# Performance work log

Measured on AMD Instinct MI355X. Metric: run time of the kernel, lower is better.

The kernel has to match this reference:

```python
import jax, jax.numpy as jnp
import numpy as np

NUM_CODES = 1024
CODE_DIM = 64
N_TOKENS = 131072
DECAY = 0.99
EPS = 1e-5


def setup_inputs() -> dict:
    key = jax.random.key(0)
    k1, k2, k3, k4 = jax.random.split(key, 4)
    return {
        "z": jax.random.normal(k1, (N_TOKENS, CODE_DIM), dtype=jnp.float32),
        "codebook": jax.random.normal(k2, (NUM_CODES, CODE_DIM), dtype=jnp.float32),
        "cluster_size": jax.random.uniform(k3, (NUM_CODES,), dtype=jnp.float32),
        "ema_w": jax.random.normal(k4, (NUM_CODES, CODE_DIM), dtype=jnp.float32),
    }


def reference(z, codebook, cluster_size, ema_w):
    # Squared L2 distances; argmin over squared distances == argmin over cdist.
    # d2: [N, K]
    d2 = (
        jnp.sum(z * z, axis=-1, keepdims=True)
        - 2.0 * (z @ codebook.T)
        + jnp.sum(codebook * codebook, axis=-1)
    )
    indices = jnp.argmin(d2, axis=-1)          # [N] int
    quantized = codebook[indices]              # [N, D]

    # EMA statistics (torch version uses one_hot; segment_sum is the fused
    # equivalent without materializing the [N, K] one-hot matrix).
    counts = jax.ops.segment_sum(jnp.ones_like(indices, dtype=z.dtype), indices,
                                 num_segments=NUM_CODES)          # encodings.sum(0)
    dw = jax.ops.segment_sum(z, indices, num_segments=NUM_CODES)  # encodings.T @ z

    new_cluster_size = DECAY * cluster_size + (1.0 - DECAY) * counts
    new_ema_w = DECAY * ema_w + (1.0 - DECAY) * dw
    n = jnp.sum(new_cluster_size)
    cs = (new_cluster_size + EPS) / (n + NUM_CODES * EPS) * n
    new_codebook = new_ema_w / cs[:, None]

    commitment_loss = jnp.mean((z - jax.lax.stop_gradient(quantized)) ** 2)
    quantized_st = z + jax.lax.stop_gradient(quantized - z)  # straight-through

    return quantized_st, indices, commitment_loss, new_codebook, new_cluster_size, new_ema_w
```

## Files before the change

### kernel.cpp

```cpp
#include <hip/hip_runtime.h>
#include <hip/hip_bf16.h>


#define DECAY 0.99f
#define OMD   0.01f
#define EPSV  1e-5f
#define BIASF 192.0f

typedef __attribute__((ext_vector_type(8))) __bf16 bf16x8;
typedef __attribute__((ext_vector_type(4))) float  float4v;

static __device__ __forceinline__ unsigned short bfbits(float f) {
    __bf16 h = (__bf16)f;
    return __builtin_bit_cast(unsigned short, h);
}
static __device__ __forceinline__ bf16x8 cvt8(float4v a, float4v b) {
    bf16x8 r;
    r[0] = (__bf16)a[0]; r[1] = (__bf16)a[1]; r[2] = (__bf16)a[2]; r[3] = (__bf16)a[3];
    r[4] = (__bf16)b[0]; r[5] = (__bf16)b[1]; r[6] = (__bf16)b[2]; r[7] = (__bf16)b[3];
    return r;
}

static __device__ __forceinline__ int dec_idx(unsigned key, int quad) {
    int iter = key & 255;
    return ((iter >> 6) << 8) + (((iter >> 2) & 15) << 4) + (quad << 2) + (iter & 3);
}

__global__ void vq_prep(const float* __restrict__ cb,
                        float* __restrict__ wsf, int* __restrict__ wsi,
                        int K, int NT) {
    int t = blockIdx.x * 256 + threadIdx.x;
    if (t < K) {
        wsi[t] = 0;
        const float4v* cp = (const float4v*)(cb + (size_t)t * 64);
        float s = 0.f;
        #pragma unroll
        for (int i = 0; i < 16; ++i) {
            float4v v = cp[i];
            s += v[0] * v[0] + v[1] * v[1] + v[2] * v[2] + v[3] * v[3];
        }
        wsf[K + t] = BIASF - 0.5f * s;
    }
    if (t == 0) wsf[2 * K] = 0.f;
}

__launch_bounds__(512)
__global__ void vq_main(const float* __restrict__ z,
                        const float* __restrict__ cb,
                        float* __restrict__ wsf, int* __restrict__ wsi,
                        float* __restrict__ out,
                        int NT, int K) {
    __shared__ __align__(16) unsigned short cbs[256 * 72];
    __shared__ float cns[256];
    __shared__ int hist[1024];

    const int tid  = threadIdx.x;
    const int lane = tid & 63;
    const int wave = tid >> 6;
    const int col  = lane & 15;
    const int quad = lane >> 4;
    const int wtok0 = blockIdx.x * 256 + wave * 32;
    const float* cnormp = wsf + K;
    float* lossp = wsf + 2 * K;
    const bool smallK = (K <= 1024);

    for (int i = tid; i < 1024; i += 512) hist[i] = 0;

    bf16x8 bf0[2], bf1[2];
    #pragma unroll
    for (int g = 0; g < 2; ++g) {
        int tok = wtok0 + g * 16 + col;
        if (tok >= NT) tok = NT - 1;
        const float* zp = z + (size_t)tok * 64 + quad * 8;
        float4v f0 = *(const float4v*)(zp);
        float4v f1 = *(const float4v*)(zp + 4);
        float4v f2 = *(const float4v*)(zp + 32);
        float4v f3 = *(const float4v*)(zp + 36);
        bf0[g] = cvt8(f0, f1);
        bf1[g] = cvt8(f2, f3);
    }

    unsigned k1[2] = { 0u, 0u }, k2[2] = { 0u, 0u };
    const unsigned kmask = 0xFFFFFF00u;
    const int nchunk = (K + 255) >> 8;

    for (int c = 0; c < nchunk; ++c) {
        #pragma unroll
        for (int i = 0; i < 8; ++i) {
            int f4 = (i * 512 + tid) * 4;
            int row = f4 >> 6, d = f4 & 63;
            int code = c * 256 + row;
            uint2 p;
            if (code < K) {
                float4v v = *(const float4v*)(cb + (size_t)code * 64 + d);
                p.x = (unsigned int)bfbits(v[0]) | ((unsigned int)bfbits(v[1]) << 16);
                p.y = (unsigned int)bfbits(v[2]) | ((unsigned int)bfbits(v[3]) << 16);
            } else { p.x = 0u; p.y = 0u; }
            *(uint2*)(&cbs[row * 72 + d]) = p;
        }
        if (tid < 256) {
            int code = c * 256 + tid;
            cns[tid] = (code < K) ? cnormp[code] : 0.0f;
        }
        __syncthreads();

        #pragma unroll 4
        for (int t = 0; t < 16; ++t) {
            const unsigned short* arow = cbs + (t * 16 + col) * 72;
            bf16x8 a0 = *(const bf16x8*)(arow + quad * 8);
            bf16x8 a1 = *(const bf16x8*)(arow + 32 + quad * 8);
            float4v cni = *(const float4v*)(cns + t * 16 + quad * 4);
            const int iterbase = (c << 6) | (t << 2);
            #pragma unroll
            for (int g = 0; g < 2; ++g) {
                float4v acc = cni;
                acc = __builtin_amdgcn_mfma_f32_16x16x32_bf16(a0, bf0[g], acc, 0, 0, 0);
                acc = __builtin_amdgcn_mfma_f32_16x16x32_bf16(a1, bf1[g], acc, 0, 0, 0);
                #pragma unroll
                for (int r = 0; r < 4; ++r) {
                    unsigned kb = (__float_as_uint(acc[r]) & kmask) | (unsigned)(iterbase + r);
                    unsigned lo = k2[g] > kb ? k2[g] : kb;
                    k2[g] = k1[g] < lo ? k1[g] : lo;
                    k1[g] = k1[g] > kb ? k1[g] : kb;
                }
            }
        }
        __syncthreads();
    }

    int ibst[2];
    #pragma unroll
    for (int g = 0; g < 2; ++g) {
        int tok = wtok0 + g * 16 + col;
        if (tok >= NT) tok = NT - 1;
        int ia = dec_idx(k1[g], quad);
        int ib = dec_idx(k2[g], quad);
        int cand[8];
        #pragma unroll
        for (int q = 0; q < 4; ++q) {
            cand[2 * q]     = __shfl(ia, q * 16 + col, 64);
            cand[2 * q + 1] = __shfl(ib, q * 16 + col, 64);
        }
        const float* zr = z + (size_t)tok * 64 + quad * 16;
        float4v zv0 = *(const float4v*)(zr);
        float4v zv1 = *(const float4v*)(zr + 4);
        float4v zv2 = *(const float4v*)(zr + 8);
        float4v zv3 = *(const float4v*)(zr + 12);
        double ps[8];
        #pragma unroll
        for (int s = 0; s < 8; ++s) {
            int cc = (cand[s] < K) ? cand[s] : 0;
            const float* cr = cb + (size_t)cc * 64 + quad * 16;
            float4v c0 = *(const float4v*)(cr);
            float4v c1 = *(const float4v*)(cr + 4);
            float4v c2 = *(const float4v*)(cr + 8);
            float4v c3 = *(const float4v*)(cr + 12);
            double a = 0.0;
            #pragma unroll
            for (int j = 0; j < 4; ++j) {
                double e0 = (double)zv0[j] - (double)c0[j];
                double e1 = (double)zv1[j] - (double)c1[j];
                double e2 = (double)zv2[j] - (double)c2[j];
                double e3 = (double)zv3[j] - (double)c3[j];
                a = fma(e0, e0, a); a = fma(e1, e1, a);
                a = fma(e2, e2, a); a = fma(e3, e3, a);
            }
            ps[s] = (cand[s] < K) ? a : 1.0e300;
        }
        #pragma unroll
        for (int s = 0; s < 8; ++s) {
            ps[s] += __shfl_xor(ps[s], 16, 64);
            ps[s] += __shfl_xor(ps[s], 32, 64);
        }
        double bs = ps[0]; int bi = cand[0];
        #pragma unroll
        for (int s = 1; s < 8; ++s) {
            if (ps[s] < bs || (ps[s] == bs && cand[s] < bi)) { bs = ps[s]; bi = cand[s]; }
        }
        ibst[g] = bi;
    }

    const size_t off_idx = (size_t)NT * 64;

    if (lane < 32) {
        int tk = wtok0 + lane;
        if (tk < NT) {
            int ib = (lane < 16) ? ibst[0] : ibst[1];
            out[off_idx + tk] = (float)ib;
            if (smallK) atomicAdd(&hist[ib], 1);
            else        atomicAdd(&wsi[ib], 1);
        }
    }

    float lsum = 0.f;
    #pragma unroll
    for (int i = 0; i < 8; ++i) {
        int tw  = i * 4 + quad;
        int g   = i >> 2;
        int idx = __shfl(ibst[g], tw & 15, 64);
        int token = wtok0 + tw;
        if (token < NT) {
            int d4 = col * 4;
            float4v zf = *(const float4v*)(z  + (size_t)token * 64 + d4);
            float4v qf = *(const float4v*)(cb + (size_t)idx   * 64 + d4);
            *(float4v*)(out + (size_t)token * 64 + d4) = qf;
            float e0 = zf[0] - qf[0], e1 = zf[1] - qf[1];
            float e2 = zf[2] - qf[2], e3 = zf[3] - qf[3];
            lsum += e0 * e0 + e1 * e1 + e2 * e2 + e3 * e3;
        }
    }
    #pragma unroll
    for (int off = 1; off < 64; off <<= 1) lsum += __shfl_xor(lsum, off, 64);
    if (lane == 0) atomicAdd(lossp, lsum);

    __syncthreads();
    if (smallK) {
        for (int k = tid; k < K; k += 512) {
            int c = hist[k];
            if (c) atomicAdd(&wsi[k], c);
        }
    }
}

__launch_bounds__(512)
__global__ void vq_dwred(const float* __restrict__ z,
                         const float* __restrict__ out_idx,
                         const float* __restrict__ cs,
                         float* __restrict__ wsf, const int* __restrict__ wsi,
                         float* __restrict__ partial,
                         float* __restrict__ out,
                         int NT, int K, int nchunks) {
    extern __shared__ float acc[];
    __shared__ float red[8];

    const int tid   = threadIdx.x;
    const int lane  = tid & 63;
    const int wave  = tid >> 6;
    const int chunk = blockIdx.x >> 2;
    const int g     = blockIdx.x & 3;
    const int tsub  = lane >> 4;
    const int d     = lane & 15;
    const size_t KD = (size_t)K * 64;

    for (int i = tid; i < K * 16; i += 512) acc[i] = 0.f;

    if (blockIdx.x == 0) {
        float part = 0.f;
        for (int k = tid; k < K; k += 512)
            part += DECAY * cs[k] + OMD * (float)wsi[k];
        #pragma unroll
        for (int off = 1; off < 64; off <<= 1) part += __shfl_xor(part, off, 64);
        if (lane == 0) red[wave] = part;
        __syncthreads();
        if (tid == 0) {
            float nn = 0.f;
            #pragma unroll
            for (int i = 0; i < 8; ++i) nn += red[i];
            wsf[2 * K + 1] = nn;
            out[(size_t)NT * 64 + NT] = wsf[2 * K] / ((float)NT * 64.0f);
        }
    }
    __syncthreads();

    const int C  = (NT + nchunks - 1) / nchunks;
    const int T0 = chunk * C;
    const int T1 = (T0 + C < NT) ? (T0 + C) : NT;
    const float* zs = z + g * 16 + d;

    #pragma unroll 4
    for (int t = T0 + wave * 4 + tsub; t < T1; t += 32) {
        float v   = zs[(size_t)t * 64];
        int  code = (int)out_idx[t];
        atomicAdd(&acc[code * 16 + d], v);
    }
    __syncthreads();

    float* pb = partial + (size_t)chunk * KD + g * 16;
    for (int i = tid; i < K * 16; i += 512) {
        int k = i >> 4, dd = i & 15;
        pb[(size_t)k * 64 + dd] = acc[i];
    }
}

__global__ void vq_final(const float* __restrict__ cs,
                         const float* __restrict__ ema,
                         const float* __restrict__ wsf,
                         const int* __restrict__ wsi,
                         const float* __restrict__ partial,
                         float* __restrict__ out, int NT, int K, int S) {
    const int KD = K * 64;
    int t = blockIdx.x * 256 + threadIdx.x;
    if (t >= KD) return;
    const int k = t >> 6;
    const float n = wsf[2 * K + 1];
    float dsum = 0.f;
    #pragma unroll 4
    for (int s = 0; s < S; ++s) dsum += partial[(size_t)s * KD + t];
    const float dw = DECAY * ema[t] + OMD * dsum;
    const float ncs = DECAY * cs[k] + OMD * (float)wsi[k];
    const float csn = (ncs + EPSV) / (n + (float)K * EPSV) * n;
    const size_t off_cb  = (size_t)NT * 64 + NT + 1;
    const size_t off_cs  = off_cb + (size_t)KD;
    const size_t off_ema = off_cs + K;
    out[off_cb  + t] = dw / csn;
    out[off_ema + t] = dw;
    if ((t & 63) == 0) out[off_cs + k] = ncs;
}

extern "C" void kernel_launch(void* const* d_in, const int* in_sizes, int n_in,
                              void* d_out, int out_size, void* d_ws, size_t ws_size,
                              hipStream_t stream) {
    const float* z   = (const float*)d_in[0];
    const float* cb  = (const float*)d_in[1];
    const float* cs  = (const float*)d_in[2];
    const float* ema = (const float*)d_in[3];
    float* out = (float*)d_out;
    float* wsf = (float*)d_ws;
    int*   wsi = (int*)d_ws;

    const int NT = in_sizes[0] / 64;
    const int K  = in_sizes[2];
    const int KD = K * 64;

    size_t avail = ws_size / 4;
    int nchunks = 128;
    while (nchunks > 1 && (size_t)2 * K + 2 + (size_t)nchunks * KD > avail)
        nchunks >>= 1;

    float* partial = wsf + 2 * K + 2;
    const size_t dwlds = (size_t)K * 16 * sizeof(float);

    vq_prep<<<(K + 255) / 256, 256, 0, stream>>>(cb, wsf, wsi, K, NT);
    vq_main<<<(NT + 255) / 256, 512, 0, stream>>>(z, cb, wsf, wsi, out, NT, K);
    vq_dwred<<<nchunks * 4, 512, dwlds, stream>>>(
        z, out + (size_t)NT * 64, cs, wsf, wsi, partial, out, NT, K, nchunks);
    vq_final<<<(KD + 255) / 256, 256, 0, stream>>>(cs, ema, wsf, wsi, partial,
                                                   out, NT, K, nchunks);
}
```

Before: 247.6 us.

## Pre-pack bf16 codebook MFMA fragments in prep kernel, read directly from global

The prep kernel now converts the codebook to bf16 once and stores it in the exact per-lane MFMA fragment layout in workspace. The main kernel drops its LDS staging of the codebook and norms, along with the per-chunk barriers, and loads each fragment straight from global/L2 inside the distance loop. This removes redundant per-block fp32-to-bf16 conversion and LDS traffic. In exchange, every wave now streams the packed codebook from cache with no LDS reuse, so the loop depends on L2 bandwidth and latency.

```diff
diff --git a/kernel.cpp b/kernel.cpp
--- a/kernel.cpp
+++ b/kernel.cpp
@@ -10,10 +10,6 @@
 typedef __attribute__((ext_vector_type(8))) __bf16 bf16x8;
 typedef __attribute__((ext_vector_type(4))) float  float4v;
 
-static __device__ __forceinline__ unsigned short bfbits(float f) {
-    __bf16 h = (__bf16)f;
-    return __builtin_bit_cast(unsigned short, h);
-}
 static __device__ __forceinline__ bf16x8 cvt8(float4v a, float4v b) {
     bf16x8 r;
     r[0] = (__bf16)a[0]; r[1] = (__bf16)a[1]; r[2] = (__bf16)a[2]; r[3] = (__bf16)a[3];
@@ -28,6 +24,7 @@
 
 __global__ void vq_prep(const float* __restrict__ cb,
                         float* __restrict__ wsf, int* __restrict__ wsi,
+                        unsigned short* __restrict__ pk,
                         int K, int NT) {
     int t = blockIdx.x * 256 + threadIdx.x;
     if (t < K) {
@@ -41,25 +38,41 @@
         }
         wsf[K + t] = BIASF - 0.5f * s;
     }
+    if (t < K * 4) {
+        int tg  = t >> 6;
+        int l   = t & 63;
+        int col = l & 15, q = l >> 4;
+        int code = tg * 16 + col;
+        bf16x8 a0, a1;
+        if (code < K) {
+            const float* s0 = cb + (size_t)code * 64 + q * 8;
+            a0 = cvt8(*(const float4v*)(s0),      *(const float4v*)(s0 + 4));
+            a1 = cvt8(*(const float4v*)(s0 + 32), *(const float4v*)(s0 + 36));
+        } else {
+            #pragma unroll
+            for (int j = 0; j < 8; ++j) { a0[j] = (__bf16)0.f; a1[j] = (__bf16)0.f; }
+        }
+        bf16x8* dst = (bf16x8*)(pk + (size_t)t * 16);
+        dst[0] = a0;
+        dst[1] = a1;
+    }
     if (t == 0) wsf[2 * K] = 0.f;
 }
 
 __launch_bounds__(512)
 __global__ void vq_main(const float* __restrict__ z,
                         const float* __restrict__ cb,
+                        const unsigned short* __restrict__ pk,
                         float* __restrict__ wsf, int* __restrict__ wsi,
                         float* __restrict__ out,
                         int NT, int K) {
-    __shared__ __align__(16) unsigned short cbs[256 * 72];
-    __shared__ float cns[256];
     __shared__ int hist[1024];
 
     const int tid  = threadIdx.x;
     const int lane = tid & 63;
-    const int wave = tid >> 6;
     const int col  = lane & 15;
     const int quad = lane >> 4;
-    const int wtok0 = blockIdx.x * 256 + wave * 32;
+    const int wtok0 = blockIdx.x * 256 + (tid >> 6) * 32;
     const float* cnormp = wsf + K;
     float* lossp = wsf + 2 * K;
     const bool smallK = (K <= 1024);
@@ -72,60 +85,35 @@
         int tok = wtok0 + g * 16 + col;
         if (tok >= NT) tok = NT - 1;
         const float* zp = z + (size_t)tok * 64 + quad * 8;
-        float4v f0 = *(const float4v*)(zp);
-        float4v f1 = *(const float4v*)(zp + 4);
-        float4v f2 = *(const float4v*)(zp + 32);
-        float4v f3 = *(const float4v*)(zp + 36);
-        bf0[g] = cvt8(f0, f1);
-        bf1[g] = cvt8(f2, f3);
+        bf0[g] = cvt8(*(const float4v*)(zp),      *(const float4v*)(zp + 4));
+        bf1[g] = cvt8(*(const float4v*)(zp + 32), *(const float4v*)(zp + 36));
     }
 
     unsigned k1[2] = { 0u, 0u }, k2[2] = { 0u, 0u };
     const unsigned kmask = 0xFFFFFF00u;
-    const int nchunk = (K + 255) >> 8;
-
-    for (int c = 0; c < nchunk; ++c) {
-        #pragma unroll
-        for (int i = 0; i < 8; ++i) {
-            int f4 = (i * 512 + tid) * 4;
-            int row = f4 >> 6, d = f4 & 63;
-            int code = c * 256 + row;
-            uint2 p;
-            if (code < K) {
-                float4v v = *(const float4v*)(cb + (size_t)code * 64 + d);
-                p.x = (unsigned int)bfbits(v[0]) | ((unsigned int)bfbits(v[1]) << 16);
-                p.y = (unsigned int)bfbits(v[2]) | ((unsigned int)bfbits(v[3]) << 16);
-            } else { p.x = 0u; p.y = 0u; }
-            *(uint2*)(&cbs[row * 72 + d]) = p;
-        }
-        if (tid < 256) {
-            int code = c * 256 + tid;
-            cns[tid] = (code < K) ? cnormp[code] : 0.0f;
-        }
-        __syncthreads();
-
-        #pragma unroll 4
-        for (int t = 0; t < 16; ++t) {
-            const unsigned short* arow = cbs + (t * 16 + col) * 72;
-            bf16x8 a0 = *(const bf16x8*)(arow + quad * 8);
-            bf16x8 a1 = *(const bf16x8*)(arow + 32 + quad * 8);
-            float4v cni = *(const float4v*)(cns + t * 16 + quad * 4);
-            const int iterbase = (c << 6) | (t << 2);
+    const int ngrp = (K + 15) >> 4;
+    const unsigned short* pl = pk + lane * 16;
+
+    #pragma unroll 2
+    for (int tt = 0; tt < ngrp; ++tt) {
+        const bf16x8* frag = (const bf16x8*)(pl + (size_t)tt * 1024);
+        bf16x8 a0 = frag[0];
+        bf16x8 a1 = frag[1];
+        float4v cni = *(const float4v*)(cnormp + tt * 16 + quad * 4);
+        const int iterbase = tt << 2;
+        #pragma unroll
+        for (int g = 0; g < 2; ++g) {
+            float4v acc = cni;
+            acc = __builtin_amdgcn_mfma_f32_16x16x32_bf16(a0, bf0[g], acc, 0, 0, 0);
+            acc = __builtin_amdgcn_mfma_f32_16x16x32_bf16(a1, bf1[g], acc, 0, 0, 0);
             #pragma unroll
-            for (int g = 0; g < 2; ++g) {
-                float4v acc = cni;
-                acc = __builtin_amdgcn_mfma_f32_16x16x32_bf16(a0, bf0[g], acc, 0, 0, 0);
-                acc = __builtin_amdgcn_mfma_f32_16x16x32_bf16(a1, bf1[g], acc, 0, 0, 0);
-                #pragma unroll
-                for (int r = 0; r < 4; ++r) {
-                    unsigned kb = (__float_as_uint(acc[r]) & kmask) | (unsigned)(iterbase + r);
-                    unsigned lo = k2[g] > kb ? k2[g] : kb;
-                    k2[g] = k1[g] < lo ? k1[g] : lo;
-                    k1[g] = k1[g] > kb ? k1[g] : kb;
-                }
+            for (int r = 0; r < 4; ++r) {
+                unsigned kb = (__float_as_uint(acc[r]) & kmask) | (unsigned)(iterbase + r);
+                unsigned lo = k2[g] > kb ? k2[g] : kb;
+                k2[g] = k1[g] < lo ? k1[g] : lo;
+                k1[g] = k1[g] > kb ? k1[g] : kb;
             }
         }
-        __syncthreads();
     }
 
     int ibst[2];
@@ -181,6 +169,7 @@
     }
 
     const size_t off_idx = (size_t)NT * 64;
+    __syncthreads();
 
     if (lane < 32) {
         int tk = wtok0 + lane;
@@ -322,16 +311,20 @@
     const int K  = in_sizes[2];
     const int KD = K * 64;
 
+    const size_t off_pk = (((size_t)2 * K + 2) + 7) & ~(size_t)7;
+    const size_t off_pa = off_pk + (size_t)K * 32;
+
     size_t avail = ws_size / 4;
     int nchunks = 128;
-    while (nchunks > 1 && (size_t)2 * K + 2 + (size_t)nchunks * KD > avail)
+    while (nchunks > 1 && off_pa + (size_t)nchunks * KD > avail)
         nchunks >>= 1;
 
-    float* partial = wsf + 2 * K + 2;
+    unsigned short* pk = (unsigned short*)(wsf + off_pk);
+    float* partial = wsf + off_pa;
     const size_t dwlds = (size_t)K * 16 * sizeof(float);
 
-    vq_prep<<<(K + 255) / 256, 256, 0, stream>>>(cb, wsf, wsi, K, NT);
-    vq_main<<<(NT + 255) / 256, 512, 0, stream>>>(z, cb, wsf, wsi, out, NT, K);
+    vq_prep<<<(K * 4 + 255) / 256, 256, 0, stream>>>(cb, wsf, wsi, pk, K, NT);
+    vq_main<<<(NT + 255) / 256, 512, 0, stream>>>(z, cb, pk, wsf, wsi, out, NT, K);
     vq_dwred<<<nchunks * 4, 512, dwlds, stream>>>(
         z, out + (size_t)NT * 64, cs, wsf, wsi, partial, out, NT, K, nchunks);
     vq_final<<<(KD + 255) / 256, 256, 0, stream>>>(cs, ema, wsf, wsi, partial,
```

Result: slower. 255.8 us (+3.3%).

## Split quantized gather and loss into separate kernel; unroll partial reduction

Applied to the files above, without the earlier changes.

The gather of codebook rows into the quantized output and the commitment-loss accumulation move out of the distance/argmin kernel into a new elementwise kernel. That kernel reads the stored indices and uses 1024-thread blocks with a block-level reduction before one atomic. The intent is to shorten the argmin kernel and lower its register and latency pressure, while giving the gather a fully coalesced layout. It costs an extra launch and a re-read of z and the indices. The final reduction over partial sums also switches to eight independent accumulators to expose more memory-level parallelism.

```diff
diff --git a/kernel.cpp b/kernel.cpp
--- a/kernel.cpp
+++ b/kernel.cpp
@@ -45,11 +45,11 @@
 }
 
 __launch_bounds__(512)
-__global__ void vq_main(const float* __restrict__ z,
-                        const float* __restrict__ cb,
-                        float* __restrict__ wsf, int* __restrict__ wsi,
-                        float* __restrict__ out,
-                        int NT, int K) {
+__global__ void vq_assign(const float* __restrict__ z,
+                          const float* __restrict__ cb,
+                          float* __restrict__ wsf, int* __restrict__ wsi,
+                          float* __restrict__ out,
+                          int NT, int K) {
     __shared__ __align__(16) unsigned short cbs[256 * 72];
     __shared__ float cns[256];
     __shared__ int hist[1024];
@@ -61,7 +61,6 @@
     const int quad = lane >> 4;
     const int wtok0 = blockIdx.x * 256 + wave * 32;
     const float* cnormp = wsf + K;
-    float* lossp = wsf + 2 * K;
     const bool smallK = (K <= 1024);
 
     for (int i = tid; i < 1024; i += 512) hist[i] = 0;
@@ -192,33 +191,47 @@
         }
     }
 
-    float lsum = 0.f;
-    #pragma unroll
-    for (int i = 0; i < 8; ++i) {
-        int tw  = i * 4 + quad;
-        int g   = i >> 2;
-        int idx = __shfl(ibst[g], tw & 15, 64);
-        int token = wtok0 + tw;
-        if (token < NT) {
-            int d4 = col * 4;
-            float4v zf = *(const float4v*)(z  + (size_t)token * 64 + d4);
-            float4v qf = *(const float4v*)(cb + (size_t)idx   * 64 + d4);
-            *(float4v*)(out + (size_t)token * 64 + d4) = qf;
-            float e0 = zf[0] - qf[0], e1 = zf[1] - qf[1];
-            float e2 = zf[2] - qf[2], e3 = zf[3] - qf[3];
-            lsum += e0 * e0 + e1 * e1 + e2 * e2 + e3 * e3;
-        }
-    }
-    #pragma unroll
-    for (int off = 1; off < 64; off <<= 1) lsum += __shfl_xor(lsum, off, 64);
-    if (lane == 0) atomicAdd(lossp, lsum);
-
     __syncthreads();
     if (smallK) {
         for (int k = tid; k < K; k += 512) {
             int c = hist[k];
             if (c) atomicAdd(&wsi[k], c);
         }
+    }
+}
+
+__launch_bounds__(1024)
+__global__ void vq_quant(const float* __restrict__ z,
+                         const float* __restrict__ cb,
+                         const float* __restrict__ out_idx,
+                         float* __restrict__ out,
+                         float* __restrict__ lossp, int NT) {
+    __shared__ float red[16];
+    const int tid  = threadIdx.x;
+    const int lane = tid & 63;
+    const int wave = tid >> 6;
+    const int gt   = blockIdx.x * 1024 + tid;
+
+    float lsum = 0.f;
+    if (gt < NT * 16) {
+        int token = gt >> 4, seg = gt & 15;
+        int idx = (int)out_idx[token];
+        const float4v zf = *(const float4v*)(z  + (size_t)token * 64 + seg * 4);
+        const float4v qf = *(const float4v*)(cb + (size_t)idx   * 64 + seg * 4);
+        *(float4v*)(out + (size_t)token * 64 + seg * 4) = qf;
+        float e0 = zf[0] - qf[0], e1 = zf[1] - qf[1];
+        float e2 = zf[2] - qf[2], e3 = zf[3] - qf[3];
+        lsum = e0 * e0 + e1 * e1 + e2 * e2 + e3 * e3;
+    }
+    #pragma unroll
+    for (int off = 1; off < 64; off <<= 1) lsum += __shfl_xor(lsum, off, 64);
+    if (lane == 0) red[wave] = lsum;
+    __syncthreads();
+    if (tid == 0) {
+        float s = 0.f;
+        #pragma unroll
+        for (int i = 0; i < 16; ++i) s += red[i];
+        atomicAdd(lossp, s);
     }
 }
 
@@ -293,9 +306,21 @@
     if (t >= KD) return;
     const int k = t >> 6;
     const float n = wsf[2 * K + 1];
-    float dsum = 0.f;
-    #pragma unroll 4
-    for (int s = 0; s < S; ++s) dsum += partial[(size_t)s * KD + t];
+    float d0 = 0.f, d1 = 0.f, d2 = 0.f, d3 = 0.f;
+    float d4 = 0.f, d5 = 0.f, d6 = 0.f, d7 = 0.f;
+    int s = 0;
+    for (; s + 8 <= S; s += 8) {
+        d0 += partial[(size_t)(s + 0) * KD + t];
+        d1 += partial[(size_t)(s + 1) * KD + t];
+        d2 += partial[(size_t)(s + 2) * KD + t];
+        d3 += partial[(size_t)(s + 3) * KD + t];
+        d4 += partial[(size_t)(s + 4) * KD + t];
+        d5 += partial[(size_t)(s + 5) * KD + t];
+        d6 += partial[(size_t)(s + 6) * KD + t];
+        d7 += partial[(size_t)(s + 7) * KD + t];
+    }
+    for (; s < S; ++s) d0 += partial[(size_t)s * KD + t];
+    const float dsum = ((d0 + d1) + (d2 + d3)) + ((d4 + d5) + (d6 + d7));
     const float dw = DECAY * ema[t] + OMD * dsum;
     const float ncs = DECAY * cs[k] + OMD * (float)wsi[k];
     const float csn = (ncs + EPSV) / (n + (float)K * EPSV) * n;
@@ -331,7 +356,9 @@
     const size_t dwlds = (size_t)K * 16 * sizeof(float);
 
     vq_prep<<<(K + 255) / 256, 256, 0, stream>>>(cb, wsf, wsi, K, NT);
-    vq_main<<<(NT + 255) / 256, 512, 0, stream>>>(z, cb, wsf, wsi, out, NT, K);
+    vq_assign<<<(NT + 255) / 256, 512, 0, stream>>>(z, cb, wsf, wsi, out, NT, K);
+    vq_quant<<<(NT * 16 + 1023) / 1024, 1024, 0, stream>>>(
+        z, cb, out + (size_t)NT * 64, out, wsf + 2 * K, NT);
     vq_dwred<<<nchunks * 4, 512, dwlds, stream>>>(
         z, out + (size_t)NT * 64, cs, wsf, wsi, partial, out, NT, K, nchunks);
     vq_final<<<(KD + 255) / 256, 256, 0, stream>>>(cs, ema, wsf, wsi, partial,
```

New measurement: 242.2 us. 1.02x faster.
